# Kernel tuning notes

Measured on AMD Instinct MI355X. Metric: run time of the kernel, lower is better.

## Reference

```python
import jax, jax.numpy as jnp
import numpy as np

D_MODEL = 192; D_STATE = 16; EXPAND = 2; D_INNER = EXPAND * D_MODEL
DT_RANK = 12  # ceil(192/16)
SG_HID = 6 * D_STATE  # SimpleGate1D expansion_factor=6
B, H, W = 4, 64, 64

def setup_inputs() -> dict:
    key = jax.random.key(0)
    ks = jax.random.split(key, 24)
    f = lambda i, shape, s=0.02: jax.random.normal(ks[i], shape, jnp.float32) * s
    # dt bias init per SS2D.dt_init: inverse-softplus of dt ~ logU(1e-3, 1e-1)
    dt = jnp.exp(jax.random.uniform(ks[20], (D_INNER,)) * (np.log(0.1) - np.log(0.001)) + np.log(0.001))
    dt = jnp.maximum(dt, 1e-4)
    inv_dt = dt + jnp.log(-jnp.expm1(-dt))
    return {
        "x": jax.random.normal(ks[0], (B, H, W, D_MODEL), jnp.float32),
        "low": jax.random.normal(ks[1], (B, H, W, D_MODEL), jnp.float32),
        "ln_g": jnp.ones((D_MODEL,), jnp.float32), "ln_b": jnp.zeros((D_MODEL,), jnp.float32),
        "in_proj_w": f(2, (2 * D_INNER, D_MODEL)),
        "in_proj_low_w": f(3, (D_INNER, D_MODEL)),
        "conv2d_w": f(4, (D_INNER, 1, 3, 3), 0.1), "conv2d_b": jnp.zeros((D_INNER,), jnp.float32),
        "x_proj_w": f(5, (DT_RANK + 2 * D_STATE, D_INNER)),
        "x_proj_w_low": f(6, (DT_RANK + 2 * D_STATE, D_INNER)),
        "conv_dt_w": f(7, (DT_RANK, 1, 15), 0.05),
        "conv_B_w": f(8, (D_STATE, 1, 15), 0.05),
        "conv_C_w": f(9, (D_STATE, 1, 15), 0.05),
        "sgb_w1": f(10, (2 * SG_HID, D_STATE), 0.1), "sgb_w2": f(11, (D_STATE, SG_HID), 0.1),
        "sgc_w1": f(12, (2 * SG_HID, D_STATE), 0.1), "sgc_w2": f(13, (D_STATE, SG_HID), 0.1),
        "dt_projs_w": f(14, (D_INNER, DT_RANK), 0.2), "dt_projs_b": inv_dt,
        "A_logs": jnp.tile(jnp.log(jnp.arange(1, D_STATE + 1, dtype=jnp.float32))[None, :], (D_INNER, 1)),
        "Ds": jnp.ones((D_INNER,), jnp.float32),
        "out_norm_g": jnp.ones((D_INNER,), jnp.float32), "out_norm_b": jnp.zeros((D_INNER,), jnp.float32),
        "out_proj_w": f(15, (D_MODEL, D_INNER)),
    }

def _ln(x, g, b):
    m = x.mean(-1, keepdims=True)
    v = x.var(-1, keepdims=True)
    return (x - m) * jax.lax.rsqrt(v + 1e-5) * g + b

def _dwconv1d(x, w, dil=2):  # x [B,C,L], w [C,1,K], depthwise, length-preserving
    pad = dil * (w.shape[-1] - 1) // 2
    return jax.lax.conv_general_dilated(x, w, (1,), [(pad, pad)], rhs_dilation=(dil,),
                                        dimension_numbers=('NCH', 'OIH', 'NCH'),
                                        feature_group_count=x.shape[1])

def _sgate(x, w1, w2):  # SimpleGate1D on [B,C,L]: fc1 -> gelu(x1)*x2 -> fc2 along C
    y = jnp.einsum('bcl,hc->bhl', x, w1)
    hid = w2.shape[1]
    g = jax.nn.gelu(y[:, :hid], approximate=False) * y[:, hid:]
    return jnp.einsum('bhl,ch->bcl', g, w2)

def _selective_scan(u, delta, A, Bs, Cs, D):
    # u,delta:[B,Di,L] A:[Di,N] Bs,Cs:[B,N,L] D:[Di]  (Mamba S6 recurrence)
    def step(h, t):
        d_t, u_t, B_t, C_t = t  # [B,Di],[B,Di],[B,N],[B,N]
        h = jnp.exp(d_t[..., None] * A) * h + (d_t * u_t)[..., None] * B_t[:, None, :]
        return h, jnp.einsum('bdn,bn->bd', h, C_t)
    h0 = jnp.zeros((u.shape[0], u.shape[1], A.shape[1]), u.dtype)
    xs = (jnp.moveaxis(delta, -1, 0), jnp.moveaxis(u, -1, 0),
          jnp.moveaxis(Bs, -1, 0), jnp.moveaxis(Cs, -1, 0))
    _, ys = jax.lax.scan(step, h0, xs)  # ys [L,B,Di]
    return jnp.moveaxis(ys, 0, -1) + u * D[:, None]

def reference(x, low, ln_g, ln_b, in_proj_w, in_proj_low_w, conv2d_w, conv2d_b,
              x_proj_w, x_proj_w_low, conv_dt_w, conv_B_w, conv_C_w,
              sgb_w1, sgb_w2, sgc_w1, sgc_w2, dt_projs_w, dt_projs_b,
              A_logs, Ds, out_norm_g, out_norm_b, out_proj_w):
    Bb, Hh, Ww, C = x.shape
    L = Hh * Ww
    R = conv_dt_w.shape[0]
    N = A_logs.shape[1]
    xn = _ln(x, ln_g, ln_b)                       # VSSBlock pre-LN
    xz = xn @ in_proj_w.T                         # [B,H,W,2*Di]
    xh, z = jnp.split(xz, 2, axis=-1)
    lowp = (low @ in_proj_low_w.T).transpose(0, 3, 1, 2)  # [B,Di,H,W]
    xc = xh.transpose(0, 3, 1, 2)
    xc = jax.lax.conv_general_dilated(xc, conv2d_w, (1, 1), [(1, 1), (1, 1)],
                                      dimension_numbers=('NCHW', 'OIHW', 'NCHW'),
                                      feature_group_count=xc.shape[1]) + conv2d_b[None, :, None, None]
    xc = jax.nn.silu(xc)
    xs = xc.reshape(Bb, -1, L)
    lows = lowp.reshape(Bb, -1, L)
    # low-branch projections (dt, B, C) with SimpleGate on B/C
    low_dbl = jnp.einsum('bdl,cd->bcl', lows, x_proj_w_low)
    dts_l, Bs_l, Cs_l = jnp.split(low_dbl, [R, R + N], axis=1)
    Bs_l = _sgate(Bs_l, sgb_w1, sgb_w2)
    Cs_l = _sgate(Cs_l, sgc_w1, sgc_w2)
    # high-branch projections
    x_dbl = jnp.einsum('bdl,cd->bcl', xs, x_proj_w)
    dts, Bs, Cs = jnp.split(x_dbl, [R, R + N], axis=1)
    dts = dts + dts_l; Bs = Bs + Bs_l; Cs = Cs + Cs_l
    # residual dilated depthwise 1D refinement of dt/B/C along L
    dts = dts + _dwconv1d(dts, conv_dt_w)
    Bs = Bs + _dwconv1d(Bs, conv_B_w)
    Cs = Cs + _dwconv1d(Cs, conv_C_w)
    delta = jax.nn.softplus(jnp.einsum('brl,dr->bdl', dts, dt_projs_w) + dt_projs_b[None, :, None])
    y = _selective_scan(xs, delta, -jnp.exp(A_logs), Bs, Cs, Ds)   # [B,Di,L]
    y = _ln(y.reshape(Bb, -1, Hh, Ww).transpose(0, 2, 3, 1), out_norm_g, out_norm_b)
    y = y * jax.nn.silu(z)
    return x + y @ out_proj_w.T  # VSSBlock residual
```

## Files before the change

### kernel.cpp

```cpp
#include <hip/hip_runtime.h>
#include <math.h>

#define LL 4096
#define NBATCH 4
#define CM 192
#define DI 384
#define NST 16
#define RK 12
#define NCH 44
#define SGH 96

typedef unsigned short ushort_t;
typedef __attribute__((ext_vector_type(8))) short bf16x8;
typedef __attribute__((ext_vector_type(4))) float f32x4;
typedef __attribute__((ext_vector_type(8))) unsigned short ushort8;
typedef __attribute__((ext_vector_type(4))) unsigned short ushort4v;

#define O_WT_IN   0
#define O_WT_LOW  147456
#define O_WT_XP   221184
#define O_WT_XPL  245760
#define O_WT_OUT  270336
#define O_XN      344064
#define O_LOWT    3489792
#define O_XH      6635520
#define O_Z       12926976
#define O_LOWP    19218432
#define O_XS      25509888
#define O_DBCH    31801344
#define O_DBCL    32522240
#define O_DBC     33243136
#define O_BS      33964032
#define O_CS      34226176
#define O_DELTA   O_LOWP
#define O_Y       O_XH
#define O_Y1      O_XN
#define O_DTS     O_DBCH

__device__ __forceinline__ ushort_t f2bf(float v) {
    unsigned u = __float_as_uint(v);
    return (ushort_t)((u + 0x7FFFu + ((u >> 16) & 1u)) >> 16);
}
__device__ __forceinline__ float bf2f(ushort_t h) {
    return __uint_as_float(((unsigned)h) << 16);
}

__device__ __forceinline__ int permidx(int l) {
    return ((l >> 2) & 3) * 1024 + ((l >> 4) << 2) + (l & 3);
}

#define LD16P(dst, row, t4) { \
  float4 _a = *(const float4*)((row) + (t4)); \
  float4 _b = *(const float4*)((row) + 1024 + (t4)); \
  float4 _c = *(const float4*)((row) + 2048 + (t4)); \
  float4 _d = *(const float4*)((row) + 3072 + (t4)); \
  dst[0]=_a.x; dst[1]=_a.y; dst[2]=_a.z; dst[3]=_a.w; \
  dst[4]=_b.x; dst[5]=_b.y; dst[6]=_b.z; dst[7]=_b.w; \
  dst[8]=_c.x; dst[9]=_c.y; dst[10]=_c.z; dst[11]=_c.w; \
  dst[12]=_d.x; dst[13]=_d.y; dst[14]=_d.z; dst[15]=_d.w; }

__global__ __launch_bounds__(256) void prep_kernel(
    const float* __restrict__ i0, ushort_t* h0, ushort_t* l0_,
    const float* __restrict__ i1, ushort_t* h1, ushort_t* l1,
    const float* __restrict__ i2, ushort_t* h2, ushort_t* l2,
    const float* __restrict__ p0, ushort_t* ph0, ushort_t* pl0,
    const float* __restrict__ p1, ushort_t* ph1, ushort_t* pl1,
    const float* __restrict__ X, const float* __restrict__ gw, const float* __restrict__ bw,
    ushort_t* __restrict__ oh, ushort_t* __restrict__ ol,
    const float* __restrict__ LOW, ushort_t* __restrict__ lh, ushort_t* __restrict__ llo)
{
    __shared__ float xt[64][193];
    __shared__ float reds[64][4], redq[64][4];
    __shared__ float mu_s[64], rs_s[64];
    int bx = blockIdx.x;
    int tid = threadIdx.x;
    if (bx < 288) {
        const float* in; ushort_t* oh_; ushort_t* ol_; int base;
        if (bx < 144)      { in = i0; oh_ = h0; ol_ = l0_; base = bx * 1024; }
        else if (bx < 216) { in = i1; oh_ = h1; ol_ = l1;  base = (bx-144) * 1024; }
        else               { in = i2; oh_ = h2; ol_ = l2;  base = (bx-216) * 1024; }
        int i = base + tid * 4;
        float4 v = *(const float4*)&in[i];
        ushort4v h, l;
        h.x = f2bf(v.x); l.x = f2bf(v.x - bf2f(h.x));
        h.y = f2bf(v.y); l.y = f2bf(v.y - bf2f(h.y));
        h.z = f2bf(v.z); l.z = f2bf(v.z - bf2f(h.z));
        h.w = f2bf(v.w); l.w = f2bf(v.w - bf2f(h.w));
        *(ushort4v*)&oh_[i] = h;
        *(ushort4v*)&ol_[i] = l;
        return;
    }
    if (bx < 336) {
        int bb = bx - 288;
        int sel = bb / 24, bxx = bb % 24;
        const float* in = sel ? p1 : p0;
        ushort_t* oh_ = sel ? ph1 : ph0;
        ushort_t* ol_ = sel ? pl1 : pl0;
        int idx = (bxx * 256 + tid) * 4;
        int n = idx / 384;
        float4 v = (n < NCH) ? *(const float4*)&in[idx] : make_float4(0.f,0.f,0.f,0.f);
        ushort4v h, l;
        h.x = f2bf(v.x); l.x = f2bf(v.x - bf2f(h.x));
        h.y = f2bf(v.y); l.y = f2bf(v.y - bf2f(h.y));
        h.z = f2bf(v.z); l.z = f2bf(v.z - bf2f(h.z));
        h.w = f2bf(v.w); l.w = f2bf(v.w - bf2f(h.w));
        *(ushort4v*)&oh_[idx] = h;
        *(ushort4v*)&ol_[idx] = l;
        return;
    }
    int ax = bx - 336;
    if (ax >= 256) {
        int i = ((ax - 256) * 256 + tid) * 4;
        float4 v = *(const float4*)&LOW[i];
        ushort4v h, l;
        h.x = f2bf(v.x); l.x = f2bf(v.x - bf2f(h.x));
        h.y = f2bf(v.y); l.y = f2bf(v.y - bf2f(h.y));
        h.z = f2bf(v.z); l.z = f2bf(v.z - bf2f(h.z));
        h.w = f2bf(v.w); l.w = f2bf(v.w - bf2f(h.w));
        *(ushort4v*)&lh[i] = h;
        *(ushort4v*)&llo[i] = l;
        return;
    }
    int t0 = ax * 64;
    const float* Xb = X + (size_t)t0 * CM;
#pragma unroll
    for (int i = 0; i < 12; i++) {
        int f4 = tid + 256 * i;
        float4 v = *(const float4*)&Xb[f4 * 4];
        int row = f4 / 48, c = (f4 % 48) * 4;
        xt[row][c] = v.x; xt[row][c+1] = v.y; xt[row][c+2] = v.z; xt[row][c+3] = v.w;
    }
    __syncthreads();
    int tok = tid & 63, p = tid >> 6;
    float s = 0.f, q = 0.f;
#pragma unroll 8
    for (int i = 0; i < 48; i++) { float v = xt[tok][p*48+i]; s += v; q = fmaf(v, v, q); }
    reds[tok][p] = s; redq[tok][p] = q;
    __syncthreads();
    if (tid < 64) {
        float ss = reds[tid][0]+reds[tid][1]+reds[tid][2]+reds[tid][3];
        float qq = redq[tid][0]+redq[tid][1]+redq[tid][2]+redq[tid][3];
        float mu = ss * (1.f/CM);
        float var = qq * (1.f/CM) - mu*mu;
        mu_s[tid] = mu; rs_s[tid] = rsqrtf(var + 1e-5f);
    }
    __syncthreads();
    int tok2 = tid >> 2, c0 = (tid & 3) * 48;
    float mu = mu_s[tok2], rs = rs_s[tok2];
    size_t tb = (size_t)(t0 + tok2) * CM;
#pragma unroll 8
    for (int i = 0; i < 48; i++) {
        int c = c0 + i;
        float v = (xt[tok2][c] - mu) * rs * gw[c] + bw[c];
        ushort_t h = f2bf(v);
        oh[tb + c] = h;
        ol[tb + c] = f2bf(v - bf2f(h));
    }
}

__global__ __launch_bounds__(256) void gemm_inlow(
    const ushort_t* __restrict__ xnh, const ushort_t* __restrict__ xnl,
    const ushort_t* __restrict__ wInH, const ushort_t* __restrict__ wInL,
    const ushort_t* __restrict__ lowh, const ushort_t* __restrict__ lowl,
    const ushort_t* __restrict__ wLowH, const ushort_t* __restrict__ wLowL,
    float* __restrict__ xh, float* __restrict__ z, float* __restrict__ lowp)
{
    __shared__ __align__(16) char smem[33280];
    ushort_t* sAh = (ushort_t*)smem;
    ushort_t* sAl = sAh + 4096;
    ushort_t* sWh = sAh + 8192;
    ushort_t* sWl = sAh + 10240;
    const int KDIM = 192;
    int tid = threadIdx.x;
    int t0 = blockIdx.x * 128;
    int b = t0 >> 12, l0 = t0 & 4095;
    int ysel = blockIdx.y;
    bool isLow = ysel >= 12;
    int n0 = (isLow ? (ysel - 12) : ysel) * 64;
    const ushort_t* Ahi = isLow ? lowh : xnh;
    const ushort_t* Alo = isLow ? lowl : xnl;
    const ushort_t* Whi = isLow ? wLowH : wInH;
    const ushort_t* Wlo = isLow ? wLowL : wInL;
    int arow = tid >> 1, kgA = (tid & 1) * 2;
    int wrow = tid >> 2, kgW = tid & 3;
    const ushort_t* gAh = Ahi + (size_t)(t0 + arow) * KDIM + kgA * 8;
    const ushort_t* gAl = Alo + (size_t)(t0 + arow) * KDIM + kgA * 8;
    const ushort_t* gWh = Whi + (size_t)(n0 + wrow) * KDIM + kgW * 8;
    const ushort_t* gWl = Wlo + (size_t)(n0 + wrow) * KDIM + kgW * 8;
    int lane = tid & 63, w = tid >> 6;
    int ln = lane & 15, kg = lane >> 4;
    int am0 = w * 32 + ln;
    f32x4 acc[2][4];
#pragma unroll
    for (int mf = 0; mf < 2; mf++)
#pragma unroll
        for (int nf = 0; nf < 4; nf++) acc[mf][nf] = (f32x4){0.f, 0.f, 0.f, 0.f};

    for (int k0 = 0; k0 < KDIM; k0 += 32) {
        __syncthreads();
        {
            ushort8 a0 = *(const ushort8*)(gAh + k0);
            ushort8 a1 = *(const ushort8*)(gAh + k0 + 8);
            *(ushort8*)(sAh + kgA*1024 + arow*8) = a0;
            *(ushort8*)(sAh + (kgA+1)*1024 + arow*8) = a1;
            ushort8 w0 = *(const ushort8*)(gWh + k0);
            *(ushort8*)(sWh + kgW*512 + wrow*8) = w0;
            ushort8 b0 = *(const ushort8*)(gAl + k0);
            ushort8 b1 = *(const ushort8*)(gAl + k0 + 8);
            *(ushort8*)(sAl + kgA*1024 + arow*8) = b0;
            *(ushort8*)(sAl + (kgA+1)*1024 + arow*8) = b1;
            ushort8 w1 = *(const ushort8*)(gWl + k0);
            *(ushort8*)(sWl + kgW*512 + wrow*8) = w1;
        }
        __syncthreads();
        bf16x8 aH[2], bH[4], aL[2], bL[4];
#pragma unroll
        for (int mf = 0; mf < 2; mf++) {
            aH[mf] = *(const bf16x8*)(sAh + kg*1024 + (am0 + mf*16)*8);
            aL[mf] = *(const bf16x8*)(sAl + kg*1024 + (am0 + mf*16)*8);
        }
#pragma unroll
        for (int nf = 0; nf < 4; nf++) {
            bH[nf] = *(const bf16x8*)(sWh + kg*512 + (nf*16 + ln)*8);
            bL[nf] = *(const bf16x8*)(sWl + kg*512 + (nf*16 + ln)*8);
        }
#pragma unroll
        for (int mf = 0; mf < 2; mf++)
#pragma unroll
            for (int nf = 0; nf < 4; nf++) {
                acc[mf][nf] = __builtin_amdgcn_mfma_f32_16x16x32_bf16(aH[mf], bH[nf], acc[mf][nf], 0, 0, 0);
                acc[mf][nf] = __builtin_amdgcn_mfma_f32_16x16x32_bf16(aH[mf], bL[nf], acc[mf][nf], 0, 0, 0);
                acc[mf][nf] = __builtin_amdgcn_mfma_f32_16x16x32_bf16(aL[mf], bH[nf], acc[mf][nf], 0, 0, 0);
            }
    }
    __syncthreads();
    float* st = (float*)smem;
#pragma unroll
    for (int mf = 0; mf < 2; mf++)
#pragma unroll
        for (int nf = 0; nf < 4; nf++)
#pragma unroll
            for (int j = 0; j < 4; j++) {
                int ml = w*32 + mf*16 + (lane>>4)*4 + j;
                int nl = nf*16 + ln;
                st[nl*130 + ml] = acc[mf][nf][j];
            }
    __syncthreads();
    int nl = tid >> 2, mq = (tid & 3) * 32;
    int n = n0 + nl;
    float* dst;
    if (!isLow) {
        dst = (n < DI) ? (xh + ((size_t)b*DI + n)*LL + l0 + mq)
                       : (z  + ((size_t)b*DI + (n - DI))*LL + l0 + mq);
    } else {
        dst = lowp + ((size_t)b*DI + n)*LL + l0 + mq;
    }
#pragma unroll
    for (int i = 0; i < 8; i++)
        *(float4*)(dst + i*4) = *(const float4*)&st[nl*130 + mq + i*4];
}

template<int MODE, int SPLIT, int PERM0>
__global__ __launch_bounds__(256) void gemm_cmaj(
    const float* __restrict__ A0, const float* __restrict__ A1,
    const ushort_t* __restrict__ W0h, const ushort_t* __restrict__ W0l,
    const ushort_t* __restrict__ W1h, const ushort_t* __restrict__ W1l,
    const float* __restrict__ resid,
    float* __restrict__ o0, float* __restrict__ o1, int Nreal)
{
    __shared__ __align__(16) char smem[33280];
    float* sA = (float*)smem;
    ushort_t* sWh = (ushort_t*)(smem + 16896);
    ushort_t* sWl = (ushort_t*)(smem + 20992);
    bool sel = (blockIdx.z == 1);
    const float* A = sel ? A1 : A0;
    const ushort_t* Wh = sel ? W1h : W0h;
    const ushort_t* Wl = sel ? W1l : W0l;
    float* out0 = sel ? o1 : o0;
    const bool perm = sel ? false : (PERM0 != 0);
    int tid = threadIdx.x;
    int t0 = blockIdx.x * 128;
    int b = t0 >> 12, l0 = t0 & 4095;
    int n0 = blockIdx.y * 64;
    const float* Ab = A + (size_t)b * 384 * LL;
    int srow = tid >> 3, sc8 = tid & 7;
    int wrow = tid >> 2, kgW = tid & 3;
    int lane = tid & 63, w = tid >> 6;
    int ln = lane & 15, kg = lane >> 4;
    int am0 = w * 32 + ln;
    f32x4 acc[2][4];
#pragma unroll
    for (int mf = 0; mf < 2; mf++)
#pragma unroll
        for (int nf = 0; nf < 4; nf++) acc[mf][nf] = (f32x4){0.f, 0.f, 0.f, 0.f};

    for (int k0 = 0; k0 < 384; k0 += 32) {
        __syncthreads();
#pragma unroll
        for (int i = 0; i < 4; i++) {
            int m = (sc8 + 8*i) * 4;
            int src = perm ? ((((m >> 2) & 3) * 1024) + (((l0 + m) >> 4) << 2))
                           : (l0 + m);
            float4 v = *(const float4*)&Ab[(size_t)(k0 + srow)*LL + src];
            *(float4*)&sA[srow*132 + m] = v;
        }
        {
            ushort8 wv = *(const ushort8*)(Wh + (size_t)(n0 + wrow)*384 + k0 + kgW*8);
            *(ushort8*)(sWh + kgW*512 + wrow*8) = wv;
            if (SPLIT == 3) {
                ushort8 wl = *(const ushort8*)(Wl + (size_t)(n0 + wrow)*384 + k0 + kgW*8);
                *(ushort8*)(sWl + kgW*512 + wrow*8) = wl;
            }
        }
        __syncthreads();
        bf16x8 aH[2], aL[2];
#pragma unroll
        for (int mf = 0; mf < 2; mf++) {
            int am = am0 + mf*16;
#pragma unroll
            for (int e = 0; e < 8; e++) {
                float v = sA[(kg*8 + e)*132 + am];
                ushort_t h = f2bf(v);
                aH[mf][e] = (short)h;
                if (SPLIT == 3) aL[mf][e] = (short)f2bf(v - bf2f(h));
            }
        }
        bf16x8 bH[4], bL[4];
#pragma unroll
        for (int nf = 0; nf < 4; nf++) {
            bH[nf] = *(const bf16x8*)(sWh + kg*512 + (nf*16 + ln)*8);
            if (SPLIT == 3) bL[nf] = *(const bf16x8*)(sWl + kg*512 + (nf*16 + ln)*8);
        }
#pragma unroll
        for (int mf = 0; mf < 2; mf++)
#pragma unroll
            for (int nf = 0; nf < 4; nf++) {
                acc[mf][nf] = __builtin_amdgcn_mfma_f32_16x16x32_bf16(aH[mf], bH[nf], acc[mf][nf], 0, 0, 0);
                if (SPLIT == 3) {
                    acc[mf][nf] = __builtin_amdgcn_mfma_f32_16x16x32_bf16(aH[mf], bL[nf], acc[mf][nf], 0, 0, 0);
                    acc[mf][nf] = __builtin_amdgcn_mfma_f32_16x16x32_bf16(aL[mf], bH[nf], acc[mf][nf], 0, 0, 0);
                }
            }
    }

    if (MODE == 2) {
#pragma unroll
        for (int mf = 0; mf < 2; mf++)
#pragma unroll
            for (int j = 0; j < 4; j++) {
                int t = t0 + w*32 + mf*16 + (lane>>4)*4 + j;
#pragma unroll
                for (int nf = 0; nf < 4; nf++) {
                    int n = n0 + nf*16 + ln;
                    out0[(size_t)t*CM + n] = resid[(size_t)t*CM + n] + acc[mf][nf][j];
                }
            }
    } else {
        __syncthreads();
        float* st = (float*)smem;
#pragma unroll
        for (int mf = 0; mf < 2; mf++)
#pragma unroll
            for (int nf = 0; nf < 4; nf++)
#pragma unroll
                for (int j = 0; j < 4; j++) {
                    int ml = w*32 + mf*16 + (lane>>4)*4 + j;
                    int nl = nf*16 + ln;
                    st[nl*130 + ml] = acc[mf][nf][j];
                }
        __syncthreads();
        int nl = tid >> 2, mq = (tid & 3) * 32;
        int n = n0 + nl;
        if (n < Nreal) {
            float* dst = out0 + ((size_t)b*Nreal + n)*LL + l0 + mq;
#pragma unroll
            for (int i = 0; i < 8; i++)
                *(float4*)(dst + i*4) = *(const float4*)&st[nl*130 + mq + i*4];
        }
    }
}

__global__ __launch_bounds__(256) void conv2d_silu_kernel(const float* __restrict__ xh,
    const float* __restrict__ w, const float* __restrict__ bias, float* __restrict__ xs)
{
    int tid = threadIdx.x;
    int l = blockIdx.x * 256 + tid;
    int c = blockIdx.y, b = blockIdx.z;
    const float* P = xh + ((size_t)b*DI + c)*LL;
    int h = l >> 6, ww = l & 63;
    float acc = bias[c];
#pragma unroll
    for (int kh = 0; kh < 3; kh++) {
        int hh = h + kh - 1;
        if ((unsigned)hh < 64u) {
#pragma unroll
            for (int kw = 0; kw < 3; kw++) {
                int wv = ww + kw - 1;
                if ((unsigned)wv < 64u) acc = fmaf(w[c*9 + kh*3 + kw], P[hh*64 + wv], acc);
            }
        }
    }
    float sg = 1.f / (1.f + __expf(-acc));
    xs[((size_t)b*DI + c)*LL + permidx(l)] = acc * sg;
}

__global__ __launch_bounds__(256) void gates_kernel(const float* __restrict__ dbcH,
    const float* __restrict__ dbcL,
    const float* __restrict__ sgb1, const float* __restrict__ sgb2,
    const float* __restrict__ sgc1, const float* __restrict__ sgc2,
    float* __restrict__ dbc)
{
    __shared__ float w1[192*16];
    __shared__ float w2[16*96];
    __shared__ float red[4][16][64];
    int tid = threadIdx.x;
    int gate = blockIdx.z;
    const float* g1 = gate ? sgc1 : sgb1;
    const float* g2 = gate ? sgc2 : sgb2;
    for (int i = tid; i < 192*16; i += 256) w1[i] = g1[i];
    for (int i = tid; i < 16*96;  i += 256) w2[i] = g2[i];
    int lq = tid & 63, p = tid >> 6;
    int l = blockIdx.x * 64 + lq;
    int b = blockIdx.y;
    size_t pb_ = (size_t)b*NCH*LL + l;
    __syncthreads();
    if (!gate) {
#pragma unroll
        for (int i = 0; i < 3; i++) {
            int c = p*3 + i;
            dbc[pb_ + (size_t)c*LL] = dbcH[pb_ + (size_t)c*LL] + dbcL[pb_ + (size_t)c*LL];
        }
    }
    int coff = RK + gate*NST;
    float xin[16], og[16];
#pragma unroll
    for (int n = 0; n < 16; n++) { xin[n] = dbcL[pb_ + (size_t)(coff+n)*LL]; og[n] = 0.f; }
    int h0 = p * 24;
    for (int h = h0; h < h0 + 24; h++) {
        float ya = 0.f, yb = 0.f;
#pragma unroll
        for (int n = 0; n < 16; n++) {
            ya = fmaf(w1[h*16+n], xin[n], ya);
            yb = fmaf(w1[(h+SGH)*16+n], xin[n], yb);
        }
        float gg = 0.5f * ya * (1.f + erff(ya * 0.70710678f)) * yb;
#pragma unroll
        for (int n = 0; n < 16; n++) og[n] = fmaf(w2[n*SGH+h], gg, og[n]);
    }
#pragma unroll
    for (int n = 0; n < 16; n++) red[p][n][lq] = og[n];
    __syncthreads();
#pragma unroll
    for (int i = 0; i < 4; i++) {
        int n = p*4 + i;
        float v = red[0][n][lq] + red[1][n][lq] + red[2][n][lq] + red[3][n][lq];
        dbc[pb_ + (size_t)(coff+n)*LL] = dbcH[pb_ + (size_t)(coff+n)*LL] + v;
    }
}

__global__ __launch_bounds__(256) void conv_dbc_kernel(const float* __restrict__ dbc,
    const float* __restrict__ wdt, const float* __restrict__ wB, const float* __restrict__ wC,
    float* __restrict__ dts, float* __restrict__ Bs, float* __restrict__ Cs)
{
    int l = blockIdx.x * 256 + threadIdx.x;
    int c = blockIdx.y, b = blockIdx.z;
    const float* wsrc = (c < RK) ? (wdt + c*15)
                      : (c < RK+NST ? wB + (c-RK)*15 : wC + (c-RK-NST)*15);
    float w[15];
#pragma unroll
    for (int k = 0; k < 15; k++) w[k] = wsrc[k];
    const float* P = dbc + ((size_t)b*NCH + c)*LL;
    float a = P[l];
#pragma unroll
    for (int k = 0; k < 15; k++) {
        int lt = l + 2*k - 14;
        if ((unsigned)lt < (unsigned)LL) a = fmaf(w[k], P[lt], a);
    }
    if (c < RK)            dts[((size_t)b*RK  + c)*LL + l] = a;
    else if (c < RK+NST)   Bs [((size_t)b*NST + (c-RK))*LL + permidx(l)] = a;
    else                   Cs [((size_t)b*NST + (c-RK-NST))*LL + permidx(l)] = a;
}

__global__ __launch_bounds__(256) void delta_kernel(const float* __restrict__ dts,
    const float* __restrict__ dtw, const float* __restrict__ dtb, float* __restrict__ delta)
{
    __shared__ float sdt[RK][128];
    __shared__ float sw[64][RK];
    int tid = threadIdx.x;
    int l0 = blockIdx.x * 128, d0 = blockIdx.y * 64, b = blockIdx.z;
    for (int i = tid; i < RK*128; i += 256) {
        int r = i >> 7, lq = i & 127;
        sdt[r][lq] = dts[((size_t)b*RK + r)*LL + l0 + lq];
    }
    for (int i = tid; i < 64*RK; i += 256) {
        int dq = i / RK, r = i - dq*RK;
        sw[dq][r] = dtw[(size_t)(d0+dq)*RK + r];
    }
    __syncthreads();
    int lq = tid & 63, g = tid >> 6;
    for (int dd = 0; dd < 16; dd++) {
        int dqq = g*16 + dd, d = d0 + dqq;
        float wr[RK];
#pragma unroll
        for (int r = 0; r < RK; r++) wr[r] = sw[dqq][r];
        float bias = dtb[d];
#pragma unroll
        for (int li = 0; li < 2; li++) {
            int lloc = lq + li*64;
            float s = bias;
#pragma unroll
            for (int r = 0; r < RK; r++) s = fmaf(wr[r], sdt[r][lloc], s);
            float sp = fmaxf(s, 0.f) + __logf(1.f + __expf(-fabsf(s)));
            delta[((size_t)b*DI + d)*LL + permidx(l0 + lloc)] = sp;
        }
    }
}

__global__ __launch_bounds__(256) void scan_kernel(
    const float* __restrict__ u_, const float* __restrict__ delta_,
    const float* __restrict__ Bs_, const float* __restrict__ Cs_,
    const float* __restrict__ Alogs, const float* __restrict__ Ds,
    float* __restrict__ y0_, float* __restrict__ y1_)
{
    __shared__ float wAs[8][4], wBs[8][4];
    __shared__ float yt[16][258];
    int tid = threadIdx.x;
    int t4 = tid * 4;
    int bid = blockIdx.x;
    int half = bid & 1, bd = bid >> 1;
    int b = bd / DI, d = bd % DI;
    int n0 = half * 8;
    size_t rowoff = ((size_t)b*DI + d)*LL;
    float dl[16], du[16], yac[16];
    LD16P(du, u_ + rowoff, t4);
    LD16P(dl, delta_ + rowoff, t4);
    float Dd = Ds[d];
#pragma unroll
    for (int s = 0; s < 16; s++) {
        yac[s] = half ? 0.f : du[s]*Dd;
        du[s] = dl[s]*du[s];
    }
    int lane = tid & 63, w = tid >> 6;
#pragma unroll 1
    for (int j = 0; j < 8; j++) {
        float An = -__expf(Alogs[d*NST + n0 + j]);
        float Bn[16], Cn[16], t[16];
        LD16P(Bn, Bs_ + ((size_t)b*NST + n0 + j)*LL, t4);
        LD16P(Cn, Cs_ + ((size_t)b*NST + n0 + j)*LL, t4);
        float a = 1.f, h = 0.f;
#pragma unroll
        for (int s = 0; s < 16; s++) {
            float e = __expf(dl[s]*An);
            a *= e;
            h = fmaf(e, h, du[s]*Bn[s]);
            yac[s] = fmaf(Cn[s], h, yac[s]);
            t[s] = Cn[s]*a;
        }
        float ap = a, hv = h;
        for (int off = 1; off < 64; off <<= 1) {
            float pa = __shfl_up(ap, (unsigned)off, 64);
            float pb = __shfl_up(hv, (unsigned)off, 64);
            if (lane >= off) { hv = fmaf(ap, pb, hv); ap *= pa; }
        }
        if (lane == 63) { wAs[j][w] = ap; wBs[j][w] = hv; }
        __syncthreads();
        float PB = 0.f;
        for (int ww = 0; ww < w; ww++) PB = fmaf(wAs[j][ww], PB, wBs[j][ww]);
        hv = fmaf(ap, PB, hv);
        float tt = __shfl_up(hv, 1u, 64);
        float hin = lane ? tt : PB;
#pragma unroll
        for (int s = 0; s < 16; s++) yac[s] = fmaf(t[s], hin, yac[s]);
    }
#pragma unroll
    for (int i = 0; i < 16; i++) yt[i][tid] = yac[i];
    __syncthreads();
    float* yout = (half ? y1_ : y0_) + rowoff;
#pragma unroll
    for (int r = 0; r < 16; r++)
        yout[r*256 + tid] = yt[tid & 15][r*16 + (tid >> 4)];
}

__global__ __launch_bounds__(1024) void outnorm_gate_kernel(const float* __restrict__ y0,
    float* y1g, const float* __restrict__ z,
    const float* __restrict__ g, const float* __restrict__ bt)
{
    __shared__ float rs_[16][64], rq_[16][64];
    __shared__ float mu_s[64], rstd_s[64];
    int tid = threadIdx.x;
    int lq = tid & 63, p = tid >> 6;
    int l = blockIdx.x * 64 + lq;
    int b = blockIdx.y;
    const float* yp0 = y0 + (size_t)b*DI*LL + l;
    float* yp1 = y1g + (size_t)b*DI*LL + l;
    float s = 0.f, q = 0.f;
#pragma unroll 4
    for (int i = 0; i < 24; i++) {
        int d = p*24 + i;
        float v = yp0[(size_t)d*LL] + yp1[(size_t)d*LL];
        s += v; q = fmaf(v, v, q);
    }
    rs_[p][lq] = s; rq_[p][lq] = q;
    __syncthreads();
    if (p == 0) {
        float ss = 0.f, qq = 0.f;
#pragma unroll
        for (int i = 0; i < 16; i++) { ss += rs_[i][lq]; qq += rq_[i][lq]; }
        float mu = ss * (1.f/DI);
        float var = qq * (1.f/DI) - mu*mu;
        mu_s[lq] = mu; rstd_s[lq] = rsqrtf(var + 1e-5f);
    }
    __syncthreads();
    float mu = mu_s[lq], rs = rstd_s[lq];
    const float* zp = z + (size_t)b*DI*LL + l;
#pragma unroll 4
    for (int i = 0; i < 24; i++) {
        int d = p*24 + i;
        float v = ((yp0[(size_t)d*LL] + yp1[(size_t)d*LL]) - mu)*rs*g[d] + bt[d];
        float zv = zp[(size_t)d*LL];
        float sg = 1.f / (1.f + __expf(-zv));
        yp1[(size_t)d*LL] = v * (zv * sg);
    }
}

extern "C" void kernel_launch(void* const* d_in, const int* in_sizes, int n_in,
                              void* d_out, int out_size, void* d_ws, size_t ws_size,
                              hipStream_t stream)
{
    (void)in_sizes; (void)n_in; (void)out_size; (void)ws_size;
    const float* x     = (const float*)d_in[0];
    const float* low   = (const float*)d_in[1];
    const float* ln_g  = (const float*)d_in[2];
    const float* ln_b  = (const float*)d_in[3];
    const float* w_in  = (const float*)d_in[4];
    const float* w_low = (const float*)d_in[5];
    const float* w_c2d = (const float*)d_in[6];
    const float* b_c2d = (const float*)d_in[7];
    const float* w_xp  = (const float*)d_in[8];
    const float* w_xpl = (const float*)d_in[9];
    const float* w_cdt = (const float*)d_in[10];
    const float* w_cB  = (const float*)d_in[11];
    const float* w_cC  = (const float*)d_in[12];
    const float* sgb1  = (const float*)d_in[13];
    const float* sgb2  = (const float*)d_in[14];
    const float* sgc1  = (const float*)d_in[15];
    const float* sgc2  = (const float*)d_in[16];
    const float* dtw   = (const float*)d_in[17];
    const float* dtb   = (const float*)d_in[18];
    const float* Alogs = (const float*)d_in[19];
    const float* Ds    = (const float*)d_in[20];
    const float* ong   = (const float*)d_in[21];
    const float* onb   = (const float*)d_in[22];
    const float* w_out = (const float*)d_in[23];
    float* ws  = (float*)d_ws;
    float* out = (float*)d_out;
    dim3 blk(256);

    ushort_t* wInH  = (ushort_t*)(ws + O_WT_IN);   ushort_t* wInL  = wInH + 147456;
    ushort_t* wLowH = (ushort_t*)(ws + O_WT_LOW);  ushort_t* wLowL = wLowH + 73728;
    ushort_t* wOutH = (ushort_t*)(ws + O_WT_OUT);  ushort_t* wOutL = wOutH + 73728;
    ushort_t* wXpH  = (ushort_t*)(ws + O_WT_XP);   ushort_t* wXpL  = wXpH + 24576;
    ushort_t* wXplH = (ushort_t*)(ws + O_WT_XPL);  ushort_t* wXplL = wXplH + 24576;
    ushort_t* xnh   = (ushort_t*)(ws + O_XN);      ushort_t* xnl   = xnh + 3145728;
    ushort_t* lowh  = (ushort_t*)(ws + O_LOWT);    ushort_t* lowl  = lowh + 3145728;

    prep_kernel<<<3664, blk, 0, stream>>>(w_in, wInH, wInL, w_low, wLowH, wLowL,
                                          w_out, wOutH, wOutL,
                                          w_xp, wXpH, wXpL, w_xpl, wXplH, wXplL,
                                          x, ln_g, ln_b, xnh, xnl, low, lowh, lowl);

    gemm_inlow<<<dim3(128,18), blk, 0, stream>>>(xnh, xnl, wInH, wInL,
                                                 lowh, lowl, wLowH, wLowL,
                                                 ws+O_XH, ws+O_Z, ws+O_LOWP);

    conv2d_silu_kernel<<<dim3(16,384,4), blk, 0, stream>>>(ws+O_XH, w_c2d, b_c2d, ws+O_XS);

    gemm_cmaj<1,3,1><<<dim3(128,1,2), blk, 0, stream>>>(ws+O_XS, ws+O_LOWP,
                                                        wXpH, wXpL, wXplH, wXplL,
                                                        nullptr, ws+O_DBCH, ws+O_DBCL, NCH);

    gates_kernel<<<dim3(64,4,2), blk, 0, stream>>>(ws+O_DBCH, ws+O_DBCL, sgb1, sgb2, sgc1, sgc2, ws+O_DBC);

    conv_dbc_kernel<<<dim3(16,44,4), blk, 0, stream>>>(ws+O_DBC, w_cdt, w_cB, w_cC,
                                                       ws+O_DTS, ws+O_BS, ws+O_CS);
    delta_kernel<<<dim3(32,6,4), blk, 0, stream>>>(ws+O_DTS, dtw, dtb, ws+O_DELTA);

    scan_kernel<<<3072, blk, 0, stream>>>(ws+O_XS, ws+O_DELTA, ws+O_BS, ws+O_CS, Alogs, Ds,
                                          ws+O_Y, ws+O_Y1);

    outnorm_gate_kernel<<<dim3(64,4), dim3(1024), 0, stream>>>(ws+O_Y, ws+O_Y1, ws+O_Z, ong, onb);

    gemm_cmaj<2,1,0><<<dim3(128,3,1), blk, 0, stream>>>(ws+O_Y1, nullptr,
                                                        wOutH, wOutL, nullptr, nullptr,
                                                        x, out, nullptr, CM);
}
```

Baseline: 259.4 us.

## Retile input and channel-major GEMMs and write MFMA accumulators directly

The input/low projection GEMM now uses 128x128 tiles (half as many blocks along N), so each loaded A tile is reused across twice as many output columns. Its shared-memory transpose epilogue is dropped in favour of direct float4 stores from the accumulators. The channel-major GEMMs shrink the token tile from 128 to 64, doubling the grid to raise occupancy and parallelism for the small-N x_proj and out_proj, and also store results directly. This trades more accumulator registers in one kernel and smaller, possibly less coalesced stores for fewer syncs and better load reuse or more blocks.

```diff
diff --git a/kernel.cpp b/kernel.cpp
--- a/kernel.cpp
+++ b/kernel.cpp
@@ -165,36 +165,35 @@
     const ushort_t* __restrict__ wLowH, const ushort_t* __restrict__ wLowL,
     float* __restrict__ xh, float* __restrict__ z, float* __restrict__ lowp)
 {
-    __shared__ __align__(16) char smem[33280];
+    __shared__ __align__(16) char smem[32768];
     ushort_t* sAh = (ushort_t*)smem;
     ushort_t* sAl = sAh + 4096;
     ushort_t* sWh = sAh + 8192;
-    ushort_t* sWl = sAh + 10240;
+    ushort_t* sWl = sAh + 12288;
     const int KDIM = 192;
     int tid = threadIdx.x;
     int t0 = blockIdx.x * 128;
     int b = t0 >> 12, l0 = t0 & 4095;
     int ysel = blockIdx.y;
-    bool isLow = ysel >= 12;
-    int n0 = (isLow ? (ysel - 12) : ysel) * 64;
+    bool isLow = ysel >= 6;
+    int n0 = (isLow ? (ysel - 6) : ysel) * 128;
     const ushort_t* Ahi = isLow ? lowh : xnh;
     const ushort_t* Alo = isLow ? lowl : xnl;
     const ushort_t* Whi = isLow ? wLowH : wInH;
     const ushort_t* Wlo = isLow ? wLowL : wInL;
     int arow = tid >> 1, kgA = (tid & 1) * 2;
-    int wrow = tid >> 2, kgW = tid & 3;
     const ushort_t* gAh = Ahi + (size_t)(t0 + arow) * KDIM + kgA * 8;
     const ushort_t* gAl = Alo + (size_t)(t0 + arow) * KDIM + kgA * 8;
-    const ushort_t* gWh = Whi + (size_t)(n0 + wrow) * KDIM + kgW * 8;
-    const ushort_t* gWl = Wlo + (size_t)(n0 + wrow) * KDIM + kgW * 8;
+    const ushort_t* gWh = Whi + (size_t)(n0 + arow) * KDIM + kgA * 8;
+    const ushort_t* gWl = Wlo + (size_t)(n0 + arow) * KDIM + kgA * 8;
     int lane = tid & 63, w = tid >> 6;
     int ln = lane & 15, kg = lane >> 4;
     int am0 = w * 32 + ln;
-    f32x4 acc[2][4];
+    f32x4 acc[2][8];
 #pragma unroll
     for (int mf = 0; mf < 2; mf++)
 #pragma unroll
-        for (int nf = 0; nf < 4; nf++) acc[mf][nf] = (f32x4){0.f, 0.f, 0.f, 0.f};
+        for (int nf = 0; nf < 8; nf++) acc[mf][nf] = (f32x4){0.f, 0.f, 0.f, 0.f};
 
     for (int k0 = 0; k0 < KDIM; k0 += 32) {
         __syncthreads();
@@ -203,61 +202,62 @@
             ushort8 a1 = *(const ushort8*)(gAh + k0 + 8);
             *(ushort8*)(sAh + kgA*1024 + arow*8) = a0;
             *(ushort8*)(sAh + (kgA+1)*1024 + arow*8) = a1;
-            ushort8 w0 = *(const ushort8*)(gWh + k0);
-            *(ushort8*)(sWh + kgW*512 + wrow*8) = w0;
             ushort8 b0 = *(const ushort8*)(gAl + k0);
             ushort8 b1 = *(const ushort8*)(gAl + k0 + 8);
             *(ushort8*)(sAl + kgA*1024 + arow*8) = b0;
             *(ushort8*)(sAl + (kgA+1)*1024 + arow*8) = b1;
-            ushort8 w1 = *(const ushort8*)(gWl + k0);
-            *(ushort8*)(sWl + kgW*512 + wrow*8) = w1;
+            ushort8 w0 = *(const ushort8*)(gWh + k0);
+            ushort8 w1 = *(const ushort8*)(gWh + k0 + 8);
+            *(ushort8*)(sWh + kgA*1024 + arow*8) = w0;
+            *(ushort8*)(sWh + (kgA+1)*1024 + arow*8) = w1;
+            ushort8 w2 = *(const ushort8*)(gWl + k0);
+            ushort8 w3 = *(const ushort8*)(gWl + k0 + 8);
+            *(ushort8*)(sWl + kgA*1024 + arow*8) = w2;
+            *(ushort8*)(sWl + (kgA+1)*1024 + arow*8) = w3;
         }
         __syncthreads();
-        bf16x8 aH[2], bH[4], aL[2], bL[4];
+        bf16x8 aH[2], aL[2];
 #pragma unroll
         for (int mf = 0; mf < 2; mf++) {
             aH[mf] = *(const bf16x8*)(sAh + kg*1024 + (am0 + mf*16)*8);
             aL[mf] = *(const bf16x8*)(sAl + kg*1024 + (am0 + mf*16)*8);
         }
 #pragma unroll
-        for (int nf = 0; nf < 4; nf++) {
-            bH[nf] = *(const bf16x8*)(sWh + kg*512 + (nf*16 + ln)*8);
-            bL[nf] = *(const bf16x8*)(sWl + kg*512 + (nf*16 + ln)*8);
-        }
-#pragma unroll
-        for (int mf = 0; mf < 2; mf++)
-#pragma unroll
-            for (int nf = 0; nf < 4; nf++) {
-                acc[mf][nf] = __builtin_amdgcn_mfma_f32_16x16x32_bf16(aH[mf], bH[nf], acc[mf][nf], 0, 0, 0);
-                acc[mf][nf] = __builtin_amdgcn_mfma_f32_16x16x32_bf16(aH[mf], bL[nf], acc[mf][nf], 0, 0, 0);
-                acc[mf][nf] = __builtin_amdgcn_mfma_f32_16x16x32_bf16(aL[mf], bH[nf], acc[mf][nf], 0, 0, 0);
+        for (int half = 0; half < 2; half++) {
+            bf16x8 bH[4], bL[4];
+#pragma unroll
+            for (int n4 = 0; n4 < 4; n4++) {
+                int nr = (half*4 + n4)*16 + ln;
+                bH[n4] = *(const bf16x8*)(sWh + kg*1024 + nr*8);
+                bL[n4] = *(const bf16x8*)(sWl + kg*1024 + nr*8);
             }
-    }
-    __syncthreads();
-    float* st = (float*)smem;
-#pragma unroll
-    for (int mf = 0; mf < 2; mf++)
-#pragma unroll
-        for (int nf = 0; nf < 4; nf++)
-#pragma unroll
-            for (int j = 0; j < 4; j++) {
-                int ml = w*32 + mf*16 + (lane>>4)*4 + j;
-                int nl = nf*16 + ln;
-                st[nl*130 + ml] = acc[mf][nf][j];
+#pragma unroll
+            for (int mf = 0; mf < 2; mf++)
+#pragma unroll
+                for (int n4 = 0; n4 < 4; n4++) {
+                    int nf = half*4 + n4;
+                    acc[mf][nf] = __builtin_amdgcn_mfma_f32_16x16x32_bf16(aH[mf], bH[n4], acc[mf][nf], 0, 0, 0);
+                    acc[mf][nf] = __builtin_amdgcn_mfma_f32_16x16x32_bf16(aH[mf], bL[n4], acc[mf][nf], 0, 0, 0);
+                    acc[mf][nf] = __builtin_amdgcn_mfma_f32_16x16x32_bf16(aL[mf], bH[n4], acc[mf][nf], 0, 0, 0);
+                }
+        }
+    }
+#pragma unroll
+    for (int mf = 0; mf < 2; mf++) {
+        int l = l0 + w*32 + mf*16 + kg*4;
+#pragma unroll
+        for (int nf = 0; nf < 8; nf++) {
+            int n = n0 + nf*16 + ln;
+            float* dst;
+            if (!isLow) {
+                dst = (n < DI) ? (xh + ((size_t)b*DI + n)*LL + l)
+                               : (z  + ((size_t)b*DI + (n - DI))*LL + l);
+            } else {
+                dst = lowp + ((size_t)b*DI + n)*LL + l;
             }
-    __syncthreads();
-    int nl = tid >> 2, mq = (tid & 3) * 32;
-    int n = n0 + nl;
-    float* dst;
-    if (!isLow) {
-        dst = (n < DI) ? (xh + ((size_t)b*DI + n)*LL + l0 + mq)
-                       : (z  + ((size_t)b*DI + (n - DI))*LL + l0 + mq);
-    } else {
-        dst = lowp + ((size_t)b*DI + n)*LL + l0 + mq;
-    }
-#pragma unroll
-    for (int i = 0; i < 8; i++)
-        *(float4*)(dst + i*4) = *(const float4*)&st[nl*130 + mq + i*4];
+            *(f32x4*)dst = acc[mf][nf];
+        }
+    }
 }
 
 template<int MODE, int SPLIT, int PERM0>
@@ -268,10 +268,9 @@
     const float* __restrict__ resid,
     float* __restrict__ o0, float* __restrict__ o1, int Nreal)
 {
-    __shared__ __align__(16) char smem[33280];
-    float* sA = (float*)smem;
-    ushort_t* sWh = (ushort_t*)(smem + 16896);
-    ushort_t* sWl = (ushort_t*)(smem + 20992);
+    __shared__ __align__(16) float sA[32*68];
+    __shared__ __align__(16) ushort_t sWh[4*64*8];
+    __shared__ __align__(16) ushort_t sWl[4*64*8];
     bool sel = (blockIdx.z == 1);
     const float* A = sel ? A1 : A0;
     const ushort_t* Wh = sel ? W1h : W0h;
@@ -279,30 +278,29 @@
     float* out0 = sel ? o1 : o0;
     const bool perm = sel ? false : (PERM0 != 0);
     int tid = threadIdx.x;
-    int t0 = blockIdx.x * 128;
+    int t0 = blockIdx.x * 64;
     int b = t0 >> 12, l0 = t0 & 4095;
     int n0 = blockIdx.y * 64;
     const float* Ab = A + (size_t)b * 384 * LL;
-    int srow = tid >> 3, sc8 = tid & 7;
     int wrow = tid >> 2, kgW = tid & 3;
     int lane = tid & 63, w = tid >> 6;
     int ln = lane & 15, kg = lane >> 4;
-    int am0 = w * 32 + ln;
-    f32x4 acc[2][4];
-#pragma unroll
-    for (int mf = 0; mf < 2; mf++)
-#pragma unroll
-        for (int nf = 0; nf < 4; nf++) acc[mf][nf] = (f32x4){0.f, 0.f, 0.f, 0.f};
+    int am0 = w * 16 + ln;
+    f32x4 acc[4];
+#pragma unroll
+    for (int nf = 0; nf < 4; nf++) acc[nf] = (f32x4){0.f, 0.f, 0.f, 0.f};
 
     for (int k0 = 0; k0 < 384; k0 += 32) {
         __syncthreads();
 #pragma unroll
-        for (int i = 0; i < 4; i++) {
-            int m = (sc8 + 8*i) * 4;
-            int src = perm ? ((((m >> 2) & 3) * 1024) + (((l0 + m) >> 4) << 2))
+        for (int i = 0; i < 2; i++) {
+            int idx = tid + 256*i;
+            int row = idx >> 4, ch = idx & 15;
+            int m = ch * 4;
+            int src = perm ? (((m >> 2) & 3) * 1024 + (((l0 + m) >> 4) << 2))
                            : (l0 + m);
-            float4 v = *(const float4*)&Ab[(size_t)(k0 + srow)*LL + src];
-            *(float4*)&sA[srow*132 + m] = v;
+            float4 v = *(const float4*)&Ab[(size_t)(k0 + row)*LL + src];
+            *(float4*)&sA[row*68 + m] = v;
         }
         {
             ushort8 wv = *(const ushort8*)(Wh + (size_t)(n0 + wrow)*384 + k0 + kgW*8);
@@ -313,17 +311,13 @@
             }
         }
         __syncthreads();
-        bf16x8 aH[2], aL[2];
-#pragma unroll
-        for (int mf = 0; mf < 2; mf++) {
-            int am = am0 + mf*16;
-#pragma unroll
-            for (int e = 0; e < 8; e++) {
-                float v = sA[(kg*8 + e)*132 + am];
-                ushort_t h = f2bf(v);
-                aH[mf][e] = (short)h;
-                if (SPLIT == 3) aL[mf][e] = (short)f2bf(v - bf2f(h));
-            }
+        bf16x8 aH, aL;
+#pragma unroll
+        for (int e = 0; e < 8; e++) {
+            float v = sA[(kg*8 + e)*68 + am0];
+            ushort_t h = f2bf(v);
+            aH[e] = (short)h;
+            if (SPLIT == 3) aL[e] = (short)f2bf(v - bf2f(h));
         }
         bf16x8 bH[4], bL[4];
 #pragma unroll
@@ -332,50 +326,32 @@
             if (SPLIT == 3) bL[nf] = *(const bf16x8*)(sWl + kg*512 + (nf*16 + ln)*8);
         }
 #pragma unroll
-        for (int mf = 0; mf < 2; mf++)
+        for (int nf = 0; nf < 4; nf++) {
+            acc[nf] = __builtin_amdgcn_mfma_f32_16x16x32_bf16(aH, bH[nf], acc[nf], 0, 0, 0);
+            if (SPLIT == 3) {
+                acc[nf] = __builtin_amdgcn_mfma_f32_16x16x32_bf16(aH, bL[nf], acc[nf], 0, 0, 0);
+                acc[nf] = __builtin_amdgcn_mfma_f32_16x16x32_bf16(aL, bH[nf], acc[nf], 0, 0, 0);
+            }
+        }
+    }
+
+    if (MODE == 2) {
+#pragma unroll
+        for (int j = 0; j < 4; j++) {
+            int t = t0 + w*16 + kg*4 + j;
 #pragma unroll
             for (int nf = 0; nf < 4; nf++) {
-                acc[mf][nf] = __builtin_amdgcn_mfma_f32_16x16x32_bf16(aH[mf], bH[nf], acc[mf][nf], 0, 0, 0);
-                if (SPLIT == 3) {
-                    acc[mf][nf] = __builtin_amdgcn_mfma_f32_16x16x32_bf16(aH[mf], bL[nf], acc[mf][nf], 0, 0, 0);
-                    acc[mf][nf] = __builtin_amdgcn_mfma_f32_16x16x32_bf16(aL[mf], bH[nf], acc[mf][nf], 0, 0, 0);
-                }
+                int n = n0 + nf*16 + ln;
+                out0[(size_t)t*CM + n] = resid[(size_t)t*CM + n] + acc[nf][j];
             }
-    }
-
-    if (MODE == 2) {
-#pragma unroll
-        for (int mf = 0; mf < 2; mf++)
-#pragma unroll
-            for (int j = 0; j < 4; j++) {
-                int t = t0 + w*32 + mf*16 + (lane>>4)*4 + j;
-#pragma unroll
-                for (int nf = 0; nf < 4; nf++) {
-                    int n = n0 + nf*16 + ln;
-                    out0[(size_t)t*CM + n] = resid[(size_t)t*CM + n] + acc[mf][nf][j];
-                }
-            }
+        }
     } else {
-        __syncthreads();
-        float* st = (float*)smem;
-#pragma unroll
-        for (int mf = 0; mf < 2; mf++)
-#pragma unroll
-            for (int nf = 0; nf < 4; nf++)
-#pragma unroll
-                for (int j = 0; j < 4; j++) {
-                    int ml = w*32 + mf*16 + (lane>>4)*4 + j;
-                    int nl = nf*16 + ln;
-                    st[nl*130 + ml] = acc[mf][nf][j];
-                }
-        __syncthreads();
-        int nl = tid >> 2, mq = (tid & 3) * 32;
-        int n = n0 + nl;
-        if (n < Nreal) {
-            float* dst = out0 + ((size_t)b*Nreal + n)*LL + l0 + mq;
-#pragma unroll
-            for (int i = 0; i < 8; i++)
-                *(float4*)(dst + i*4) = *(const float4*)&st[nl*130 + mq + i*4];
+        int l = l0 + w*16 + kg*4;
+#pragma unroll
+        for (int nf = 0; nf < 4; nf++) {
+            int n = n0 + nf*16 + ln;
+            if (n < Nreal)
+                *(f32x4*)(out0 + ((size_t)b*Nreal + n)*LL + l) = acc[nf];
         }
     }
 }
@@ -669,13 +645,13 @@
                                           w_xp, wXpH, wXpL, w_xpl, wXplH, wXplL,
                                           x, ln_g, ln_b, xnh, xnl, low, lowh, lowl);
 
-    gemm_inlow<<<dim3(128,18), blk, 0, stream>>>(xnh, xnl, wInH, wInL,
-                                                 lowh, lowl, wLowH, wLowL,
-                                                 ws+O_XH, ws+O_Z, ws+O_LOWP);
+    gemm_inlow<<<dim3(128,9), blk, 0, stream>>>(xnh, xnl, wInH, wInL,
+                                                lowh, lowl, wLowH, wLowL,
+                                                ws+O_XH, ws+O_Z, ws+O_LOWP);
 
     conv2d_silu_kernel<<<dim3(16,384,4), blk, 0, stream>>>(ws+O_XH, w_c2d, b_c2d, ws+O_XS);
 
-    gemm_cmaj<1,3,1><<<dim3(128,1,2), blk, 0, stream>>>(ws+O_XS, ws+O_LOWP,
+    gemm_cmaj<1,3,1><<<dim3(256,1,2), blk, 0, stream>>>(ws+O_XS, ws+O_LOWP,
                                                         wXpH, wXpL, wXplH, wXplL,
                                                         nullptr, ws+O_DBCH, ws+O_DBCL, NCH);
 
@@ -690,7 +666,7 @@
 
     outnorm_gate_kernel<<<dim3(64,4), dim3(1024), 0, stream>>>(ws+O_Y, ws+O_Y1, ws+O_Z, ong, onb);
 
-    gemm_cmaj<2,1,0><<<dim3(128,3,1), blk, 0, stream>>>(ws+O_Y1, nullptr,
+    gemm_cmaj<2,1,0><<<dim3(256,3,1), blk, 0, stream>>>(ws+O_Y1, nullptr,
                                                         wOutH, wOutL, nullptr, nullptr,
                                                         x, out, nullptr, CM);
 }
```

Result: faster. 235.1 us (-9.4%).
